# Optimization experiments

Hardware: AMD Instinct MI355X
Metric: run time of the kernel (lower is better)

Reference implementation:

```python
import jax, jax.numpy as jnp
import numpy as np

N_NODES = 100000
N_EDGES = 1600000
D_IN = 128
HID = 32
HEADS = 4
D_OUT = 40
NEG_SLOPE = 0.2


def edge_softmax(scores, dst, n_nodes):
    # scores: [E, H]; softmax over incoming edges of each destination node
    m = jax.ops.segment_max(scores, dst, num_segments=n_nodes)  # [N, H]
    e = jnp.exp(scores - m[dst])
    s = jax.ops.segment_sum(e, dst, num_segments=n_nodes)  # [N, H]
    return e / s[dst]


def gat_conv(x, src, dst, W, attn_l, attn_r, bias):
    # x: [N, Din]; W: [Din, H*F]; attn_l/attn_r: [H, F]; bias: [H*F]
    n = x.shape[0]
    h = (x @ W).reshape(n, HEADS, HID)          # [N, H, F]
    el = jnp.einsum('nhf,hf->nh', h, attn_l)    # [N, H]
    er = jnp.einsum('nhf,hf->nh', h, attn_r)    # [N, H]
    e = jax.nn.leaky_relu(el[src] + er[dst], NEG_SLOPE)  # [E, H]
    a = edge_softmax(e, dst, n)                 # [E, H]
    msg = h[src] * a[:, :, None]                # [E, H, F]
    out = jax.ops.segment_sum(msg, dst, num_segments=n)  # [N, H, F]
    return out + bias.reshape(HEADS, HID)


def setup_inputs() -> dict:
    key = jax.random.key(0)
    ks = jax.random.split(key, 12)
    x = jax.random.normal(ks[0], (N_NODES, D_IN), dtype=jnp.float32)
    src = jax.random.randint(ks[1], (N_EDGES,), 0, N_NODES, dtype=jnp.int32)
    dst = jax.random.randint(ks[2], (N_EDGES,), 0, N_NODES, dtype=jnp.int32)
    s = 0.05
    W1 = jax.random.normal(ks[3], (D_IN, HEADS * HID), dtype=jnp.float32) * s
    al1 = jax.random.normal(ks[4], (HEADS, HID), dtype=jnp.float32) * s
    ar1 = jax.random.normal(ks[5], (HEADS, HID), dtype=jnp.float32) * s
    b1 = jnp.zeros((HEADS * HID,), dtype=jnp.float32)
    W2 = jax.random.normal(ks[6], (HEADS * HID, HEADS * HID), dtype=jnp.float32) * s
    al2 = jax.random.normal(ks[7], (HEADS, HID), dtype=jnp.float32) * s
    ar2 = jax.random.normal(ks[8], (HEADS, HID), dtype=jnp.float32) * s
    b2 = jnp.zeros((HEADS * HID,), dtype=jnp.float32)
    Wout = jax.random.normal(ks[9], (HEADS * HID, D_OUT), dtype=jnp.float32) * s
    bout = jnp.zeros((D_OUT,), dtype=jnp.float32)
    return {"x": x, "src": src, "dst": dst,
            "W1": W1, "al1": al1, "ar1": ar1, "b1": b1,
            "W2": W2, "al2": al2, "ar2": ar2, "b2": b2,
            "Wout": Wout, "bout": bout}


def reference(x, src, dst, W1, al1, ar1, b1, W2, al2, ar2, b2, Wout, bout):
    n = x.shape[0]
    h = gat_conv(x, src, dst, W1, al1, ar1, b1).reshape(n, -1)  # flatten(1)
    h = jax.nn.elu(h)
    h = gat_conv(h, src, dst, W2, al2, ar2, b2).reshape(n, -1)
    h = jax.nn.elu(h)
    return h @ Wout + bout  # final Linear, flatten(1) is a no-op on 2D
```

## Files before the change

kernel.cpp:

```cpp
#include <hip/hip_runtime.h>
#include <hip/hip_fp16.h>
#include <math.h>

#define N_NODES 100000
#define N_EDGES 1600000
#define NEG_SLOPE 0.2f

#define NB ((N_NODES + 255) / 256)
#define NC 1024
#define CHUNK ((N_EDGES + NC - 1) / NC)

#define WT_STRIDE 136
#define CS_STRIDE 136

typedef _Float16 f16x2 __attribute__((ext_vector_type(2)));
typedef _Float16 f16x4 __attribute__((ext_vector_type(4)));
typedef float f32x4v __attribute__((ext_vector_type(4)));

#define MFMA16(a, b, c) __builtin_amdgcn_mfma_f32_16x16x16f16(a, b, c, 0, 0, 0)

__device__ __forceinline__ float lrelu(float x) { return x > 0.f ? x : NEG_SLOPE * x; }
__device__ __forceinline__ float eluf(float x)  { return x > 0.f ? x : expm1f(x); }


__global__ __launch_bounds__(256) void p1_hist(const int* __restrict__ dst,
                                               int* __restrict__ H) {
  __shared__ int hist[NB];
  int c = blockIdx.x, t = threadIdx.x;
  for (int i = t; i < NB; i += 256) hist[i] = 0;
  __syncthreads();
  int e0 = c * CHUNK, e1 = min(e0 + CHUNK, N_EDGES);
  for (int e = e0 + t; e < e1; e += 256) atomicAdd(&hist[dst[e] >> 8], 1);
  __syncthreads();
  for (int i = t; i < NB; i += 256) H[i * NC + c] = hist[i];
}

__global__ __launch_bounds__(256) void p2_colscan(int* __restrict__ H,
                                                  int* __restrict__ colTotal) {
  __shared__ int sh[256];
  int b = blockIdx.x, t = threadIdx.x;
  int4 v = *(int4*)&H[b * NC + t * 4];
  int tsum = v.x + v.y + v.z + v.w;
  sh[t] = tsum;
  __syncthreads();
  for (int off = 1; off < 256; off <<= 1) {
    int u = (t >= off) ? sh[t - off] : 0;
    __syncthreads();
    sh[t] += u;
    __syncthreads();
  }
  int excl = sh[t] - tsum;
  int4 o;
  o.x = excl;
  o.y = excl + v.x;
  o.z = o.y + v.y;
  o.w = o.z + v.z;
  *(int4*)&H[b * NC + t * 4] = o;
  if (t == 255) colTotal[b] = sh[255];
}

__global__ __launch_bounds__(512) void p3_bucketscan(const int* __restrict__ colTotal,
                                                     int* __restrict__ bucketBase) {
  __shared__ int sh[512];
  int t = threadIdx.x;
  int v = (t < NB) ? colTotal[t] : 0;
  sh[t] = v;
  __syncthreads();
  for (int off = 1; off < 512; off <<= 1) {
    int u = (t >= off) ? sh[t - off] : 0;
    __syncthreads();
    sh[t] += u;
    __syncthreads();
  }
  if (t < NB) bucketBase[t] = sh[t] - v;
  if (t == NB - 1) bucketBase[NB] = sh[t];
}

__global__ __launch_bounds__(256) void p4_scatter(const int* __restrict__ src,
                                                  const int* __restrict__ dst,
                                                  const int* __restrict__ H,
                                                  const int* __restrict__ bucketBase,
                                                  int* __restrict__ tmp) {
  __shared__ int cur[NB];
  int c = blockIdx.x, t = threadIdx.x;
  for (int i = t; i < NB; i += 256) cur[i] = bucketBase[i] + H[i * NC + c];
  __syncthreads();
  int e0 = c * CHUNK, e1 = min(e0 + CHUNK, N_EDGES);
  for (int e = e0 + t; e < e1; e += 256) {
    int d = dst[e];
    int pos = atomicAdd(&cur[d >> 8], 1);
    tmp[pos] = (src[e] << 8) | (d & 255);
  }
}

__global__ __launch_bounds__(256) void p5_build(const int* __restrict__ tmp,
                                                const int* __restrict__ bucketBase,
                                                int* __restrict__ rowstart,
                                                int* __restrict__ csr_src) {
  __shared__ int hist[256];
  __shared__ int sh[256];
  __shared__ int cur[256];
  int b = blockIdx.x, t = threadIdx.x;
  int ebase = bucketBase[b], eend = bucketBase[b + 1];
  hist[t] = 0;
  __syncthreads();
  for (int e = ebase + t; e < eend; e += 256) atomicAdd(&hist[tmp[e] & 255], 1);
  __syncthreads();
  int v = hist[t];
  sh[t] = v;
  __syncthreads();
  for (int off = 1; off < 256; off <<= 1) {
    int u = (t >= off) ? sh[t - off] : 0;
    __syncthreads();
    sh[t] += u;
    __syncthreads();
  }
  int excl = sh[t] - v;
  int node = b * 256 + t;
  if (node < N_NODES) rowstart[node] = ebase + excl;
  cur[t] = excl;
  __syncthreads();
  for (int e = ebase + t; e < eend; e += 256) {
    int p = tmp[e];
    int pos = ebase + atomicAdd(&cur[p & 255], 1);
    csr_src[pos] = p >> 8;
  }
  if (b == 0 && t == 0) rowstart[N_NODES] = N_EDGES;
}

template <bool FP16IN>
__global__ __launch_bounds__(256) void gemm128_mfma(const void* __restrict__ Av,
                                                    const float* __restrict__ W,
                                                    const float* __restrict__ al,
                                                    const float* __restrict__ ar,
                                                    __half* __restrict__ C,
                                                    float* __restrict__ el,
                                                    float* __restrict__ er, int N) {
  __shared__ _Float16 WtCs[128 * WT_STRIDE];
  __shared__ float als[128], ars[128];
  int tid = threadIdx.x;
  int wv = tid >> 6;
  int l = tid & 63;
  int li = l & 15, lk = l >> 4;
  int rowBase = blockIdx.x * 64;

  if (tid < 128) { als[tid] = al[tid]; ars[tid] = ar[tid]; }

#pragma unroll 4
  for (int i = 0; i < 32; i++) {
    int idx = tid + 256 * i;
    int c = idx & 127, k = (idx >> 7) * 2;
    f16x2 p;
    p[0] = (_Float16)W[k * 128 + c];
    p[1] = (_Float16)W[(k + 1) * 128 + c];
    *(f16x2*)&WtCs[c * WT_STRIDE + k] = p;
  }

  f16x4 afr[8];
  int ra = min(rowBase + wv * 16 + li, N - 1);
  if constexpr (FP16IN) {
    const _Float16* A = (const _Float16*)Av;
#pragma unroll
    for (int ch = 0; ch < 8; ch++)
      afr[ch] = *(const f16x4*)&A[(size_t)ra * 128 + ch * 16 + lk * 4];
  } else {
    const float* A = (const float*)Av;
#pragma unroll
    for (int ch = 0; ch < 8; ch++) {
      float4 v = *(const float4*)&A[(size_t)ra * 128 + ch * 16 + lk * 4];
      f16x4 a;
      a[0] = (_Float16)v.x; a[1] = (_Float16)v.y;
      a[2] = (_Float16)v.z; a[3] = (_Float16)v.w;
      afr[ch] = a;
    }
  }
  __syncthreads();

  f32x4v acc[8];
#pragma unroll
  for (int ct = 0; ct < 8; ct++) acc[ct] = (f32x4v){0.f, 0.f, 0.f, 0.f};

#pragma unroll
  for (int ch = 0; ch < 8; ch++) {
#pragma unroll
    for (int ct = 0; ct < 8; ct++) {
      f16x4 b = *(const f16x4*)&WtCs[(ct * 16 + li) * WT_STRIDE + ch * 16 + lk * 4];
      acc[ct] = MFMA16(afr[ch], b, acc[ct]);
    }
  }

  float alc[8], arc[8];
#pragma unroll
  for (int ct = 0; ct < 8; ct++) {
    alc[ct] = als[ct * 16 + li];
    arc[ct] = ars[ct * 16 + li];
  }
#pragma unroll
  for (int j = 0; j < 4; j++) {
    float el4[4], er4[4];
#pragma unroll
    for (int hh = 0; hh < 4; hh++) {
      el4[hh] = acc[2 * hh][j] * alc[2 * hh] + acc[2 * hh + 1][j] * alc[2 * hh + 1];
      er4[hh] = acc[2 * hh][j] * arc[2 * hh] + acc[2 * hh + 1][j] * arc[2 * hh + 1];
    }
#pragma unroll
    for (int m = 1; m < 16; m <<= 1) {
#pragma unroll
      for (int hh = 0; hh < 4; hh++) {
        el4[hh] += __shfl_xor(el4[hh], m, 64);
        er4[hh] += __shfl_xor(er4[hh], m, 64);
      }
    }
    int row = rowBase + wv * 16 + lk * 4 + j;
    if (li == 0 && row < N) {
      *(float4*)&el[row * 4] = make_float4(el4[0], el4[1], el4[2], el4[3]);
      *(float4*)&er[row * 4] = make_float4(er4[0], er4[1], er4[2], er4[3]);
    }
  }

  __syncthreads();
#pragma unroll
  for (int j = 0; j < 4; j++) {
    int rl = wv * 16 + lk * 4 + j;
#pragma unroll
    for (int ct = 0; ct < 8; ct++)
      WtCs[rl * CS_STRIDE + ct * 16 + li] = (_Float16)acc[ct][j];
  }
  __syncthreads();
  int rrow = tid >> 2, ckk = tid & 3;
  int grow = rowBase + rrow;
  if (grow < N) {
#pragma unroll
    for (int q = 0; q < 4; q++) {
      float4 v = *(float4*)&WtCs[rrow * CS_STRIDE + ckk * 32 + q * 8];
      *(float4*)&C[(size_t)grow * 128 + ckk * 32 + q * 8] = v;
    }
  }
}

__global__ __launch_bounds__(256) void agg_fused(const __half* __restrict__ h,
                                                 const float* __restrict__ el,
                                                 const float* __restrict__ er,
                                                 const int* __restrict__ rowstart,
                                                 const int* __restrict__ csr_src,
                                                 const float* __restrict__ bias,
                                                 __half* __restrict__ out) {
  __shared__ float wlds[16][17][4];
  __shared__ int   ilds[16][17];
  int tid = threadIdx.x;
  int slot = tid >> 4;
  int l = tid & 15;
  int n = blockIdx.x * 16 + slot;
  if (n >= N_NODES) return;
  int base = rowstart[n];
  int deg = rowstart[n + 1] - base;
  int f0 = l * 8;
  int head = l >> 2;
  float acc[8] = {};
  float lsum = 0.f;

  if (deg > 0) {
    float4 erv = *(const float4*)&er[n * 4];

    for (int t0 = 0; t0 < deg; t0 += 16) {
      int e = t0 + l;
      bool act = e < deg;
      int s = act ? csr_src[base + e] : 0;
      float4 elv = *(const float4*)&el[s * 4];
      float w0 = act ? __expf(fminf(lrelu(elv.x + erv.x), 30.f)) : 0.f;
      float w1 = act ? __expf(fminf(lrelu(elv.y + erv.y), 30.f)) : 0.f;
      float w2 = act ? __expf(fminf(lrelu(elv.z + erv.z), 30.f)) : 0.f;
      float w3 = act ? __expf(fminf(lrelu(elv.w + erv.w), 30.f)) : 0.f;
      *(float4*)&wlds[slot][l][0] = make_float4(w0, w1, w2, w3);
      ilds[slot][l] = s;
      __builtin_amdgcn_wave_barrier();

      int nt = min(16, deg - t0);
#pragma unroll 4
      for (int i = 0; i < nt; i++) {
        int si = ilds[slot][i];
        float wi = wlds[slot][i][head];
        lsum += wi;
        float4 raw = *(const float4*)&h[(size_t)si * 128 + f0];
        const __half2* hp = (const __half2*)&raw;
        float2 c0 = __half22float2(hp[0]);
        float2 c1 = __half22float2(hp[1]);
        float2 c2 = __half22float2(hp[2]);
        float2 c3 = __half22float2(hp[3]);
        acc[0] = fmaf(c0.x, wi, acc[0]); acc[1] = fmaf(c0.y, wi, acc[1]);
        acc[2] = fmaf(c1.x, wi, acc[2]); acc[3] = fmaf(c1.y, wi, acc[3]);
        acc[4] = fmaf(c2.x, wi, acc[4]); acc[5] = fmaf(c2.y, wi, acc[5]);
        acc[6] = fmaf(c3.x, wi, acc[6]); acc[7] = fmaf(c3.y, wi, acc[7]);
      }
      __builtin_amdgcn_wave_barrier();
    }
    float rh = 1.f / lsum;
#pragma unroll
    for (int j = 0; j < 8; j++) acc[j] *= rh;
  }
  float4 b0 = *(const float4*)&bias[f0];
  float4 b1 = *(const float4*)&bias[f0 + 4];
  float r0 = eluf(acc[0] + b0.x), r1 = eluf(acc[1] + b0.y);
  float r2 = eluf(acc[2] + b0.z), r3 = eluf(acc[3] + b0.w);
  float r4 = eluf(acc[4] + b1.x), r5 = eluf(acc[5] + b1.y);
  float r6 = eluf(acc[6] + b1.z), r7 = eluf(acc[7] + b1.w);
  __half2 pk[4];
  pk[0] = __float22half2_rn(make_float2(r0, r1));
  pk[1] = __float22half2_rn(make_float2(r2, r3));
  pk[2] = __float22half2_rn(make_float2(r4, r5));
  pk[3] = __float22half2_rn(make_float2(r6, r7));
  *(float4*)&out[(size_t)n * 128 + f0] = *(float4*)pk;
}

__global__ __launch_bounds__(256) void gemm_out_k(const __half* __restrict__ A,
                                                  const float* __restrict__ Wo,
                                                  const float* __restrict__ bo,
                                                  float* __restrict__ C, int N) {
  __shared__ float As[64 * 132];
  __shared__ float Ws[128 * 44];
  int tid = threadIdx.x;
  int rowBase = blockIdx.x * 64;
  for (int i = tid; i < 128 * 40; i += 256) {
    int r = i / 40, c = i % 40;
    Ws[r * 44 + c] = Wo[i];
  }
#pragma unroll
  for (int j = 0; j < 4; j++) {
    int v = tid + 256 * j;
    int r = v >> 4, c8 = (v & 15) * 8;
    int gr = min(rowBase + r, N - 1);
    float4 raw = *(const float4*)&A[(size_t)gr * 128 + c8];
    const __half2* hp = (const __half2*)&raw;
    float2 f0 = __half22float2(hp[0]);
    float2 f1 = __half22float2(hp[1]);
    float2 f2 = __half22float2(hp[2]);
    float2 f3 = __half22float2(hp[3]);
    float* dstp = &As[r * 132 + c8];
    dstp[0] = f0.x; dstp[1] = f0.y; dstp[2] = f1.x; dstp[3] = f1.y;
    dstp[4] = f2.x; dstp[5] = f2.y; dstp[6] = f3.x; dstp[7] = f3.y;
  }
  __syncthreads();
  int rg = tid >> 4, cg = tid & 15;
  if (cg < 10) {
    float acc[4][4] = {};
#pragma unroll 4
    for (int k = 0; k < 128; k++) {
      float a[4];
#pragma unroll
      for (int i = 0; i < 4; i++) a[i] = As[(rg + 16 * i) * 132 + k];
      float4 w = *(const float4*)&Ws[k * 44 + cg * 4];
#pragma unroll
      for (int i = 0; i < 4; i++) {
        acc[i][0] = fmaf(a[i], w.x, acc[i][0]);
        acc[i][1] = fmaf(a[i], w.y, acc[i][1]);
        acc[i][2] = fmaf(a[i], w.z, acc[i][2]);
        acc[i][3] = fmaf(a[i], w.w, acc[i][3]);
      }
    }
    float4 bv = *(const float4*)&bo[cg * 4];
#pragma unroll
    for (int i = 0; i < 4; i++) {
      int r = rowBase + rg + 16 * i;
      if (r < N) {
        float4 o = make_float4(acc[i][0] + bv.x, acc[i][1] + bv.y,
                               acc[i][2] + bv.z, acc[i][3] + bv.w);
        *(float4*)&C[r * 40 + cg * 4] = o;
      }
    }
  }
}

extern "C" void kernel_launch(void* const* d_in, const int* in_sizes, int n_in,
                              void* d_out, int out_size, void* d_ws, size_t ws_size,
                              hipStream_t stream) {
  const float* x    = (const float*)d_in[0];
  const int*   src  = (const int*)d_in[1];
  const int*   dst  = (const int*)d_in[2];
  const float* W1   = (const float*)d_in[3];
  const float* al1  = (const float*)d_in[4];
  const float* ar1  = (const float*)d_in[5];
  const float* b1   = (const float*)d_in[6];
  const float* W2   = (const float*)d_in[7];
  const float* al2  = (const float*)d_in[8];
  const float* ar2  = (const float*)d_in[9];
  const float* b2   = (const float*)d_in[10];
  const float* Wout = (const float*)d_in[11];
  const float* bout = (const float*)d_in[12];
  float* out = (float*)d_out;

  const int N = N_NODES, E = N_EDGES;
  size_t off = 0;
  auto alloc = [&](size_t bytes) {
    void* p = (char*)d_ws + off;
    off += (bytes + 255) & ~(size_t)255;
    return p;
  };
  __half* hh  = (__half*)alloc((size_t)N * 128 * 2);
  __half* o16 = (__half*)alloc((size_t)N * 128 * 2);
  float* el  = (float*)alloc((size_t)N * 4 * 4);
  float* er  = (float*)alloc((size_t)N * 4 * 4);
  int* rowstart   = (int*)alloc((size_t)(N + 1) * 4);
  int* H          = (int*)alloc((size_t)NB * NC * 4);
  int* colTotal   = (int*)alloc((size_t)NB * 4);
  int* bucketBase = (int*)alloc((size_t)(NB + 1) * 4);
  int* tmp        = (int*)alloc((size_t)E * 4);
  int* csr_src    = (int*)alloc((size_t)E * 4);
  (void)ws_size; (void)in_sizes; (void)n_in; (void)out_size;

  p1_hist<<<NC, 256, 0, stream>>>(dst, H);
  p2_colscan<<<NB, 256, 0, stream>>>(H, colTotal);
  p3_bucketscan<<<1, 512, 0, stream>>>(colTotal, bucketBase);
  p4_scatter<<<NC, 256, 0, stream>>>(src, dst, H, bucketBase, tmp);
  p5_build<<<NB, 256, 0, stream>>>(tmp, bucketBase, rowstart, csr_src);

  int gemmGrid = (N + 63) / 64;
  int outGrid  = (N + 63) / 64;
  int aggGrid  = (N + 15) / 16;

  gemm128_mfma<false><<<gemmGrid, 256, 0, stream>>>(x, W1, al1, ar1, hh, el, er, N);
  agg_fused<<<aggGrid, 256, 0, stream>>>(hh, el, er, rowstart, csr_src, b1, o16);

  gemm128_mfma<true><<<gemmGrid, 256, 0, stream>>>(o16, W2, al2, ar2, hh, el, er, N);
  agg_fused<<<aggGrid, 256, 0, stream>>>(hh, el, er, rowstart, csr_src, b2, o16);

  gemm_out_k<<<outGrid, 256, 0, stream>>>(o16, Wout, bout, out, N);
}
```

Before: 283.3 us.

## Halve CSR bucket width and move output GEMM to fp16 MFMA

```diff
diff --git a/kernel.cpp b/kernel.cpp
--- a/kernel.cpp
+++ b/kernel.cpp
@@ -6,7 +6,8 @@
 #define N_EDGES 1600000
 #define NEG_SLOPE 0.2f
 
-#define NB ((N_NODES + 255) / 256)
+#define BKT 128
+#define NB ((N_NODES + BKT - 1) / BKT)
 #define NC 1024
 #define CHUNK ((N_EDGES + NC - 1) / NC)
 
@@ -30,7 +31,7 @@
   for (int i = t; i < NB; i += 256) hist[i] = 0;
   __syncthreads();
   int e0 = c * CHUNK, e1 = min(e0 + CHUNK, N_EDGES);
-  for (int e = e0 + t; e < e1; e += 256) atomicAdd(&hist[dst[e] >> 8], 1);
+  for (int e = e0 + t; e < e1; e += 256) atomicAdd(&hist[dst[e] >> 7], 1);
   __syncthreads();
   for (int i = t; i < NB; i += 256) H[i * NC + c] = hist[i];
 }
@@ -59,14 +60,14 @@
   if (t == 255) colTotal[b] = sh[255];
 }
 
-__global__ __launch_bounds__(512) void p3_bucketscan(const int* __restrict__ colTotal,
-                                                     int* __restrict__ bucketBase) {
-  __shared__ int sh[512];
+__global__ __launch_bounds__(1024) void p3_bucketscan(const int* __restrict__ colTotal,
+                                                      int* __restrict__ bucketBase) {
+  __shared__ int sh[1024];
   int t = threadIdx.x;
   int v = (t < NB) ? colTotal[t] : 0;
   sh[t] = v;
   __syncthreads();
-  for (int off = 1; off < 512; off <<= 1) {
+  for (int off = 1; off < 1024; off <<= 1) {
     int u = (t >= off) ? sh[t - off] : 0;
     __syncthreads();
     sh[t] += u;
@@ -88,8 +89,8 @@
   int e0 = c * CHUNK, e1 = min(e0 + CHUNK, N_EDGES);
   for (int e = e0 + t; e < e1; e += 256) {
     int d = dst[e];
-    int pos = atomicAdd(&cur[d >> 8], 1);
-    tmp[pos] = (src[e] << 8) | (d & 255);
+    int pos = atomicAdd(&cur[d >> 7], 1);
+    tmp[pos] = (src[e] << 7) | (d & 127);
   }
 }
 
@@ -97,33 +98,35 @@
                                                 const int* __restrict__ bucketBase,
                                                 int* __restrict__ rowstart,
                                                 int* __restrict__ csr_src) {
-  __shared__ int hist[256];
-  __shared__ int sh[256];
-  __shared__ int cur[256];
+  __shared__ int hist[BKT];
+  __shared__ int sh[BKT];
+  __shared__ int cur[BKT];
   int b = blockIdx.x, t = threadIdx.x;
   int ebase = bucketBase[b], eend = bucketBase[b + 1];
-  hist[t] = 0;
-  __syncthreads();
-  for (int e = ebase + t; e < eend; e += 256) atomicAdd(&hist[tmp[e] & 255], 1);
-  __syncthreads();
-  int v = hist[t];
-  sh[t] = v;
-  __syncthreads();
-  for (int off = 1; off < 256; off <<= 1) {
-    int u = (t >= off) ? sh[t - off] : 0;
-    __syncthreads();
-    sh[t] += u;
-    __syncthreads();
-  }
-  int excl = sh[t] - v;
-  int node = b * 256 + t;
-  if (node < N_NODES) rowstart[node] = ebase + excl;
-  cur[t] = excl;
+  if (t < BKT) hist[t] = 0;
+  __syncthreads();
+  for (int e = ebase + t; e < eend; e += 256) atomicAdd(&hist[tmp[e] & (BKT - 1)], 1);
+  __syncthreads();
+  int v = (t < BKT) ? hist[t] : 0;
+  if (t < BKT) sh[t] = v;
+  __syncthreads();
+  for (int off = 1; off < BKT; off <<= 1) {
+    int u = (t >= off && t < BKT) ? sh[t - off] : 0;
+    __syncthreads();
+    if (t < BKT) sh[t] += u;
+    __syncthreads();
+  }
+  if (t < BKT) {
+    int excl = sh[t] - v;
+    int node = b * BKT + t;
+    if (node < N_NODES) rowstart[node] = ebase + excl;
+    cur[t] = excl;
+  }
   __syncthreads();
   for (int e = ebase + t; e < eend; e += 256) {
     int p = tmp[e];
-    int pos = ebase + atomicAdd(&cur[p & 255], 1);
-    csr_src[pos] = p >> 8;
+    int pos = ebase + atomicAdd(&cur[p & (BKT - 1)], 1);
+    csr_src[pos] = p >> 7;
   }
   if (b == 0 && t == 0) rowstart[N_NODES] = N_EDGES;
 }
@@ -316,55 +319,53 @@
                                                   const float* __restrict__ Wo,
                                                   const float* __restrict__ bo,
                                                   float* __restrict__ C, int N) {
-  __shared__ float As[64 * 132];
-  __shared__ float Ws[128 * 44];
+  __shared__ _Float16 WoT[48 * WT_STRIDE];
   int tid = threadIdx.x;
+  int wv = tid >> 6;
+  int l = tid & 63;
+  int li = l & 15, lk = l >> 4;
   int rowBase = blockIdx.x * 64;
-  for (int i = tid; i < 128 * 40; i += 256) {
-    int r = i / 40, c = i % 40;
-    Ws[r * 44 + c] = Wo[i];
-  }
-#pragma unroll
-  for (int j = 0; j < 4; j++) {
-    int v = tid + 256 * j;
-    int r = v >> 4, c8 = (v & 15) * 8;
-    int gr = min(rowBase + r, N - 1);
-    float4 raw = *(const float4*)&A[(size_t)gr * 128 + c8];
-    const __half2* hp = (const __half2*)&raw;
-    float2 f0 = __half22float2(hp[0]);
-    float2 f1 = __half22float2(hp[1]);
-    float2 f2 = __half22float2(hp[2]);
-    float2 f3 = __half22float2(hp[3]);
-    float* dstp = &As[r * 132 + c8];
-    dstp[0] = f0.x; dstp[1] = f0.y; dstp[2] = f1.x; dstp[3] = f1.y;
-    dstp[4] = f2.x; dstp[5] = f2.y; dstp[6] = f3.x; dstp[7] = f3.y;
-  }
-  __syncthreads();
-  int rg = tid >> 4, cg = tid & 15;
-  if (cg < 10) {
-    float acc[4][4] = {};
-#pragma unroll 4
-    for (int k = 0; k < 128; k++) {
-      float a[4];
-#pragma unroll
-      for (int i = 0; i < 4; i++) a[i] = As[(rg + 16 * i) * 132 + k];
-      float4 w = *(const float4*)&Ws[k * 44 + cg * 4];
-#pragma unroll
-      for (int i = 0; i < 4; i++) {
-        acc[i][0] = fmaf(a[i], w.x, acc[i][0]);
-        acc[i][1] = fmaf(a[i], w.y, acc[i][1]);
-        acc[i][2] = fmaf(a[i], w.z, acc[i][2]);
-        acc[i][3] = fmaf(a[i], w.w, acc[i][3]);
-      }
-    }
-    float4 bv = *(const float4*)&bo[cg * 4];
-#pragma unroll
-    for (int i = 0; i < 4; i++) {
-      int r = rowBase + rg + 16 * i;
-      if (r < N) {
-        float4 o = make_float4(acc[i][0] + bv.x, acc[i][1] + bv.y,
-                               acc[i][2] + bv.z, acc[i][3] + bv.w);
-        *(float4*)&C[r * 40 + cg * 4] = o;
+
+#pragma unroll
+  for (int i = 0; i < 12; i++) {
+    int idx = tid + 256 * i;
+    int c = idx >> 6, k2 = (idx & 63) * 2;
+    f16x2 p;
+    p[0] = (c < 40) ? (_Float16)Wo[k2 * 40 + c] : (_Float16)0.f;
+    p[1] = (c < 40) ? (_Float16)Wo[(k2 + 1) * 40 + c] : (_Float16)0.f;
+    *(f16x2*)&WoT[c * WT_STRIDE + k2] = p;
+  }
+
+  f16x4 afr[8];
+  int ra = min(rowBase + wv * 16 + li, N - 1);
+  const _Float16* Ah = (const _Float16*)A;
+#pragma unroll
+  for (int ch = 0; ch < 8; ch++)
+    afr[ch] = *(const f16x4*)&Ah[(size_t)ra * 128 + ch * 16 + lk * 4];
+  __syncthreads();
+
+  f32x4v acc[3];
+#pragma unroll
+  for (int ct = 0; ct < 3; ct++) acc[ct] = (f32x4v){0.f, 0.f, 0.f, 0.f};
+
+#pragma unroll
+  for (int ch = 0; ch < 8; ch++) {
+#pragma unroll
+    for (int ct = 0; ct < 3; ct++) {
+      f16x4 b = *(const f16x4*)&WoT[(ct * 16 + li) * WT_STRIDE + ch * 16 + lk * 4];
+      acc[ct] = MFMA16(afr[ch], b, acc[ct]);
+    }
+  }
+
+#pragma unroll
+  for (int ct = 0; ct < 3; ct++) {
+    int col = ct * 16 + li;
+    if (col < 40) {
+      float bv = bo[col];
+#pragma unroll
+      for (int j = 0; j < 4; j++) {
+        int row = rowBase + wv * 16 + lk * 4 + j;
+        if (row < N) C[(size_t)row * 40 + col] = acc[ct][j] + bv;
       }
     }
   }
@@ -409,7 +410,7 @@
 
   p1_hist<<<NC, 256, 0, stream>>>(dst, H);
   p2_colscan<<<NB, 256, 0, stream>>>(H, colTotal);
-  p3_bucketscan<<<1, 512, 0, stream>>>(colTotal, bucketBase);
+  p3_bucketscan<<<1, 1024, 0, stream>>>(colTotal, bucketBase);
   p4_scatter<<<NC, 256, 0, stream>>>(src, dst, H, bucketBase, tmp);
   p5_build<<<NB, 256, 0, stream>>>(tmp, bucketBase, rowstart, csr_src);
 
```

New measurement: 287.5 us. No clear change (+1.5%).
